# Kernel tuning notes

Hardware: AMD Instinct MI355X
Metric: run time of the kernel (lower is better)

The kernel has to match this reference:

```python
import jax, jax.numpy as jnp
import numpy as np

B, ENC, DEC, H, OUT = 4096, 168, 24, 64, 1
IN = 1 + 5 + 3 + 4 + 7  # 20


def _lstm_step(xt, h, c, Wih, Whh, bih, bhh):
    # PyTorch gate order: i, f, g, o
    g = xt @ Wih.T + h @ Whh.T + bih + bhh
    i, f, gg, o = jnp.split(g, 4, axis=-1)
    c = jax.nn.sigmoid(f) * c + jax.nn.sigmoid(i) * jnp.tanh(gg)
    h = jax.nn.sigmoid(o) * jnp.tanh(c)
    return h, c


def _lstm_layer(x, Wih, Whh, bih, bhh):
    # x: [T, B, in] -> ys: [T, B, H], final (h, c)
    h0 = jnp.zeros((x.shape[1], Whh.shape[1]), x.dtype)

    def step(carry, xt):
        h, c = _lstm_step(xt, carry[0], carry[1], Wih, Whh, bih, bhh)
        return (h, c), h

    (h, c), ys = jax.lax.scan(step, (h0, h0), x)
    return ys, h, c


def setup_inputs() -> dict:
    key = jax.random.key(0)
    ks = jax.random.split(key, 24)
    rn = lambda k, s, sc=0.05: jax.random.normal(k, s, jnp.float32) * sc
    inp = {
        "input_p_q": rn(ks[0], (B, ENC, 1), 1.0),
        "input_time": jax.random.randint(ks[1], (B, ENC, 4), 0, 8),
        "label_p": rn(ks[2], (B, ENC), 1.0),
        "decoder_time": jax.random.randint(ks[3], (B, DEC, 4), 0, 8),
        # encoder LSTM layer 0
        "enc0_Wih": rn(ks[4], (4 * H, IN)), "enc0_Whh": rn(ks[5], (4 * H, H)),
        "enc0_bih": rn(ks[6], (4 * H,)), "enc0_bhh": rn(ks[7], (4 * H,)),
        # encoder LSTM layer 1
        "enc1_Wih": rn(ks[8], (4 * H, H)), "enc1_Whh": rn(ks[9], (4 * H, H)),
        "enc1_bih": rn(ks[10], (4 * H,)), "enc1_bhh": rn(ks[11], (4 * H,)),
        # decoder LSTMCell (input = OUT + 19 = 20)
        "dec_Wih": rn(ks[12], (4 * H, OUT + 19)), "dec_Whh": rn(ks[13], (4 * H, H)),
        "dec_bih": rn(ks[14], (4 * H,)), "dec_bhh": rn(ks[15], (4 * H,)),
        # output projection
        "Wout": rn(ks[16], (OUT, H)), "bout": rn(ks[17], (OUT,)),
        # embeddings
        "emb_hour": rn(ks[18], (24, 5)), "emb_wd": rn(ks[19], (8, 3)),
        "emb_mo": rn(ks[20], (13, 4)), "emb_woy": rn(ks[21], (54, 7)),
    }
    return inp


def reference(input_p_q, input_time, label_p, decoder_time,
              enc0_Wih, enc0_Whh, enc0_bih, enc0_bhh,
              enc1_Wih, enc1_Whh, enc1_bih, enc1_bhh,
              dec_Wih, dec_Whh, dec_bih, dec_bhh,
              Wout, bout, emb_hour, emb_wd, emb_mo, emb_woy):
    def time_feats(t):  # t: [B, T, 4] int -> [B, T, 19]
        return jnp.concatenate([emb_hour[t[:, :, 0]], emb_wd[t[:, :, 1]],
                                emb_mo[t[:, :, 2]], emb_woy[t[:, :, 3]]], axis=-1)

    input_q = label_p[:, :ENC, None]                      # [B, ENC, 1]
    enc_in = jnp.concatenate([input_q, time_feats(input_time)], axis=-1)  # [B, ENC, 20]
    x = enc_in.transpose(1, 0, 2)                         # [ENC, B, 20]
    ys0, _, _ = _lstm_layer(x, enc0_Wih, enc0_Whh, enc0_bih, enc0_bhh)
    _, h1, c1 = _lstm_layer(ys0, enc1_Wih, enc1_Whh, enc1_bih, enc1_bhh)

    dec_feat = time_feats(decoder_time).transpose(1, 0, 2)  # [DEC, B, 19]
    prev0 = label_p[:, ENC - 1, None]                       # [B, 1]

    def dec_step(carry, ft):
        h, c, prev = carry
        xin = jnp.concatenate([prev, ft], axis=-1)          # [B, 20]
        h, c = _lstm_step(xin, h, c, dec_Wih, dec_Whh, dec_bih, dec_bhh)
        out = h @ Wout.T + bout                             # [B, OUT]
        return (h, c, out), out

    _, outs = jax.lax.scan(dec_step, (h1, c1, prev0), dec_feat)
    return outs.transpose(1, 0, 2)                          # [B, DEC, OUT]
```

## Files before the change

### kernel.cpp

```cpp
#include <hip/hip_runtime.h>

#define DEVFN __device__ __forceinline__

typedef float  f32x4  __attribute__((ext_vector_type(4)));
typedef short  bf16x8 __attribute__((ext_vector_type(8)));

constexpr int ENC = 168;
constexpr int DEC = 24;
constexpr int BT  = 16;
constexpr int NBLK = 4096 / BT;

constexpr int W0F = 0;
constexpr int W1F = 24576;
constexpr int WDF = 57344;
constexpr int F_B0   = 40960;
constexpr int F_B1   = 41216;
constexpr int F_BD   = 41472;
constexpr int F_WOUT = 41728;
constexpr int F_BOUT = 41792;
constexpr int F_EMB  = 41793;
constexpr int NEMB = 574;

DEVFN ushort f2bf(float v) {
    unsigned b = __float_as_uint(v);
    return (ushort)((b + 0x7FFFu + ((b >> 16) & 1u)) >> 16);
}
DEVFN float bf2f(ushort u) { return __uint_as_float(((unsigned)u) << 16); }
DEVFN float sigm(float x)  { return __builtin_amdgcn_rcpf(1.f + __expf(-x)); }
DEVFN float tanhv(float x) { return fmaf(2.f, sigm(x + x), -1.f); }

DEVFN unsigned cvt_pk_bf16(float a, float b) {
    unsigned r;
    asm("v_cvt_pk_bf16_f32 %0, %1, %2" : "=v"(r) : "v"(a), "v"(b));
    return r;
}

DEVFN void pinv(bf16x8& v) { asm volatile("" : "+v"(v)); }
DEVFN void pinf(f32x4& v)  { asm volatile("" : "+v"(v)); }

__global__ void prep_kernel(
    const float* __restrict__ w0ih, const float* __restrict__ w0hh,
    const float* __restrict__ b0ih, const float* __restrict__ b0hh,
    const float* __restrict__ w1ih, const float* __restrict__ w1hh,
    const float* __restrict__ b1ih, const float* __restrict__ b1hh,
    const float* __restrict__ wdih, const float* __restrict__ wdhh,
    const float* __restrict__ bdih, const float* __restrict__ bdhh,
    const float* __restrict__ wout, const float* __restrict__ boutp,
    const float* __restrict__ eh,   const float* __restrict__ ewd,
    const float* __restrict__ emo,  const float* __restrict__ ewoy,
    void* __restrict__ ws)
{
    ushort* wsu = (ushort*)ws;
    float*  wsf = (float*)ws;
    const int total = 81920 + 1407;
    for (int idx = blockIdx.x * blockDim.x + threadIdx.x; idx < total;
         idx += gridDim.x * blockDim.x) {
        if (idx < 81920) {
            int layer, q;
            if (idx < W1F)      { layer = 0; q = idx; }
            else if (idx < WDF) { layer = 1; q = idx - W1F; }
            else                { layer = 2; q = idx - WDF; }
            int c  = q >> 13;
            int tt = (q >> 9) & 15;
            int l  = (q >> 3) & 63;
            int j  = q & 7;
            int k  = c * 32 + (l >> 4) * 8 + j;
            int n  = tt * 16 + (l & 15);
            float v = 0.f;
            if (layer == 0) {
                if (k < 20) v = w0ih[n * 20 + k];
                else if (k < 84) v = w0hh[n * 64 + (k - 20)];
            } else if (layer == 1) {
                if (k < 64) v = w1ih[n * 64 + k];
                else        v = w1hh[n * 64 + (k - 64)];
            } else {
                if (k < 20) v = wdih[n * 20 + k];
                else if (k < 84) v = wdhh[n * 64 + (k - 20)];
            }
            wsu[idx] = f2bf(v);
        } else {
            int f = idx - 81920;
            float v;
            if (f < 256)      v = b0ih[f] + b0hh[f];
            else if (f < 512) v = b1ih[f - 256] + b1hh[f - 256];
            else if (f < 768) v = bdih[f - 512] + bdhh[f - 512];
            else if (f < 832) v = wout[f - 768];
            else if (f == 832) v = boutp[0];
            else {
                int e = f - 833;
                if (e < 120)      v = eh[e];
                else if (e < 144) v = ewd[e - 120];
                else if (e < 196) v = emo[e - 144];
                else              v = ewoy[e - 196];
            }
            wsf[40960 + f] = v;
        }
    }
}

DEVFN float emb_lookup(const float* s_emb, int kk, int idx) {
    int f = kk - 1;
    if (f < 5)  return s_emb[idx * 5 + f];
    if (f < 8)  return s_emb[120 + idx * 3 + (f - 5)];
    if (f < 12) return s_emb[144 + idx * 4 + (f - 8)];
    return s_emb[196 + idx * 7 + (f - 12)];
}

DEVFN int offC0(int k, int m) {
    int c = k >> 5, k32 = k & 31;
    return c * 512 + (m + 16 * (k32 >> 3)) * 8 + (k32 & 7);
}
DEVFN int offC3(int k, int m) {
    int c = 3 + (k >> 5), k32 = k & 31;
    return c * 512 + (m + 16 * (k32 >> 3)) * 8 + (k32 & 7);
}
DEVFN void store_h(ushort* A, int off, float h) {
    A[off] = f2bf(h);
}
DEVFN void store_h4(ushort* A, int off, const float* h) {
    unsigned h01 = cvt_pk_bf16(h[0], h[1]);
    unsigned h23 = cvt_pk_bf16(h[2], h[3]);
    asm volatile("" : "+v"(h01), "+v"(h23));
    unsigned long long p = ((unsigned long long)h23 << 32) | h01;
    *(unsigned long long*)(A + off) = p;
}

__global__ __launch_bounds__(512)
__attribute__((amdgpu_waves_per_eu(2, 2)))
void lstm_mfma(
    const int* __restrict__ input_time, const float* __restrict__ label_p,
    const int* __restrict__ decoder_time, const void* __restrict__ ws,
    float* __restrict__ out)
{
    const ushort* wsu = (const ushort*)ws;
    const float*  wsf = (const float*)ws;

    __shared__ __align__(16) ushort Abuf[2][7 * 512];
    __shared__ float s_emb[NEMB];
    __shared__ float s_wout[64];
    __shared__ float sh1[16 * 68];
    __shared__ float s_bout;

    const int tid = threadIdx.x;
    const int w   = tid >> 6;
    const int l   = tid & 63;
    const int q   = l >> 4;
    const int m   = l & 15;
    const int wl  = w & 3;
    const bool isL0 = (w < 4);
    const int b0g = blockIdx.x * BT;
    const int u0  = wl * 16 + q * 4;

    for (int i = tid; i < 2 * 7 * 512; i += 512) ((ushort*)Abuf)[i] = 0;
    for (int i = tid; i < NEMB; i += 512) s_emb[i] = wsf[F_EMB + i];
    if (tid < 64) s_wout[tid] = wsf[F_WOUT + tid];
    if (tid == 0) s_bout = wsf[F_BOUT];

    bf16x8 wA[4][4];
    if (isL0) {
#pragma unroll
        for (int c = 0; c < 3; c++)
#pragma unroll
            for (int g = 0; g < 4; g++)
                wA[c][g] = *(const bf16x8*)(wsu + W0F +
                    (c * 16 + g * 4 + wl) * 512 + l * 8);
        wA[3][0] = wA[3][1] = wA[3][2] = wA[3][3] = bf16x8{0,0,0,0,0,0,0,0};
    } else {
#pragma unroll
        for (int c = 0; c < 4; c++)
#pragma unroll
            for (int g = 0; g < 4; g++)
                wA[c][g] = *(const bf16x8*)(wsu + W1F +
                    (c * 16 + g * 4 + wl) * 512 + l * 8);
    }
#pragma unroll
    for (int c = 0; c < 4; c++)
#pragma unroll
        for (int g = 0; g < 4; g++) pinv(wA[c][g]);

    f32x4 biasv[4];
#pragma unroll
    for (int g = 0; g < 4; g++) {
        biasv[g] = *(const f32x4*)(wsf + (isL0 ? F_B0 : F_B1) + g * 64 + u0);
        pinf(biasv[g]);
    }

    float cst[4] = {0.f, 0.f, 0.f, 0.f};

    const int kk = tid >> 4, mm = tid & 15;
    const bool bx = (tid < 320);
    const int sel = (kk <= 5) ? 0 : (kk <= 8) ? 1 : (kk <= 12) ? 2 : 3;

    __syncthreads();
    if (bx) {
        float v = (kk == 0) ? label_p[(b0g + mm) * ENC]
                : emb_lookup(s_emb, kk, input_time[((b0g + mm) * ENC) * 4 + sel]);
        store_h(Abuf[0], offC0(kk, mm), v);
    }
    __syncthreads();

    for (int i = 0; i <= ENC; ++i) {
        const ushort* Ar = Abuf[i & 1];
        ushort* Aw = Abuf[(i + 1) & 1];
        const bool active = isL0 ? (i < ENC) : (i >= 1);

        float pre_f = 0.f; int pre_i = 0;
        const bool encX  = (i + 1 < ENC) && bx;
        const bool decX0 = (i == ENC) && bx;
        if (encX) {
            if (kk == 0) pre_f = label_p[(b0g + mm) * ENC + (i + 1)];
            else         pre_i = input_time[((b0g + mm) * ENC + (i + 1)) * 4 + sel];
        } else if (decX0) {
            if (kk == 0) pre_f = label_p[(b0g + mm) * ENC + (ENC - 1)];
            else         pre_i = decoder_time[((b0g + mm) * DEC) * 4 + sel];
        }

        if (active) {
            f32x4 acc[4];
#pragma unroll
            for (int g = 0; g < 4; g++) acc[g] = biasv[g];
            if (isL0) {
                bf16x8 ah[3];
#pragma unroll
                for (int c = 0; c < 3; c++)
                    ah[c] = *(const bf16x8*)(Ar + c * 512 + l * 8);
#pragma unroll
                for (int c = 0; c < 3; c++)
#pragma unroll
                    for (int g = 0; g < 4; g++)
                        acc[g] = __builtin_amdgcn_mfma_f32_16x16x32_bf16(
                            wA[c][g], ah[c], acc[g], 0, 0, 0);
            } else {
                bf16x8 ah[4];
#pragma unroll
                for (int c = 0; c < 4; c++)
                    ah[c] = *(const bf16x8*)(Ar + (3 + c) * 512 + l * 8);
#pragma unroll
                for (int c = 0; c < 4; c++)
#pragma unroll
                    for (int g = 0; g < 4; g++)
                        acc[g] = __builtin_amdgcn_mfma_f32_16x16x32_bf16(
                            wA[c][g], ah[c], acc[g], 0, 0, 0);
            }
            float hv[4];
#pragma unroll
            for (int r = 0; r < 4; r++) {
                float cc = sigm(acc[1][r]) * cst[r] + sigm(acc[0][r]) * tanhv(acc[2][r]);
                cst[r] = cc;
                hv[r] = sigm(acc[3][r]) * tanhv(cc);
            }
            if (isL0) {
                store_h4(Aw, offC3(u0, m), hv);
                store_h4(Aw, offC0(20 + u0, m), hv);
            } else {
                if (i < ENC) store_h4(Aw, offC3(64 + u0, m), hv);
                else         store_h4(Aw, offC0(20 + u0, m), hv);
            }
        }
        if (encX || decX0)
            store_h(Aw, offC0(kk, mm), (kk == 0) ? pre_f : emb_lookup(s_emb, kk, pre_i));
        __syncthreads();
    }

    if (!isL0) {
#pragma unroll
        for (int c = 0; c < 3; c++)
#pragma unroll
            for (int g = 0; g < 4; g++)
                wA[c][g] = *(const bf16x8*)(wsu + WDF +
                    (c * 16 + g * 4 + wl) * 512 + l * 8);
#pragma unroll
        for (int c = 0; c < 3; c++)
#pragma unroll
            for (int g = 0; g < 4; g++) pinv(wA[c][g]);
#pragma unroll
        for (int g = 0; g < 4; g++) {
            biasv[g] = *(const f32x4*)(wsf + F_BD + g * 64 + u0);
            pinf(biasv[g]);
        }
    }

    for (int t = 0; t < DEC; ++t) {
        const ushort* Ar = Abuf[(t + 1) & 1];
        ushort* Aw = Abuf[t & 1];

        int pre_i = 0;
        const bool dX = (t + 1 < DEC) && bx && (kk >= 1);
        if (dX) pre_i = decoder_time[((b0g + mm) * DEC + (t + 1)) * 4 + sel];

        if (!isL0) {
            bf16x8 ah[3];
#pragma unroll
            for (int c = 0; c < 3; c++)
                ah[c] = *(const bf16x8*)(Ar + c * 512 + l * 8);
            f32x4 acc[4];
#pragma unroll
            for (int g = 0; g < 4; g++) acc[g] = biasv[g];
#pragma unroll
            for (int c = 0; c < 3; c++)
#pragma unroll
                for (int g = 0; g < 4; g++)
                    acc[g] = __builtin_amdgcn_mfma_f32_16x16x32_bf16(
                        wA[c][g], ah[c], acc[g], 0, 0, 0);
            float hv[4];
#pragma unroll
            for (int r = 0; r < 4; r++) {
                float cc = sigm(acc[1][r]) * cst[r] + sigm(acc[0][r]) * tanhv(acc[2][r]);
                cst[r] = cc;
                hv[r] = sigm(acc[3][r]) * tanhv(cc);
            }
            store_h4(Aw, offC0(20 + u0, m), hv);
            *(f32x4*)&sh1[m * 68 + u0] = *(f32x4*)hv;
        }
        if (dX) store_h(Aw, offC0(kk, mm), emb_lookup(s_emb, kk, pre_i));
        __syncthreads();

        if (tid < 16) {
            float a = s_bout;
#pragma unroll 16
            for (int u = 0; u < 64; u++) a = fmaf(s_wout[u], sh1[tid * 68 + u], a);
            out[(b0g + tid) * DEC + t] = a;
            if (t + 1 < DEC) store_h(Aw, offC0(0, tid), a);
        }
        __syncthreads();
    }
}

extern "C" void kernel_launch(void* const* d_in, const int* in_sizes, int n_in,
                              void* d_out, int out_size, void* d_ws, size_t ws_size,
                              hipStream_t stream)
{
    typedef const float* fp;
    const int* input_time   = (const int*)d_in[1];
    fp         label_p      = (fp)d_in[2];
    const int* decoder_time = (const int*)d_in[3];

    prep_kernel<<<128, 256, 0, stream>>>(
        (fp)d_in[4],  (fp)d_in[5],  (fp)d_in[6],  (fp)d_in[7],
        (fp)d_in[8],  (fp)d_in[9],  (fp)d_in[10], (fp)d_in[11],
        (fp)d_in[12], (fp)d_in[13], (fp)d_in[14], (fp)d_in[15],
        (fp)d_in[16], (fp)d_in[17],
        (fp)d_in[18], (fp)d_in[19], (fp)d_in[20], (fp)d_in[21],
        d_ws);

    lstm_mfma<<<NBLK, 512, 0, stream>>>(
        input_time, label_p, decoder_time, d_ws, (float*)d_out);
}
```

Before: 303.5 us.

## Fold log2e into gate weights, fuse LSTM cell math, share h buffer layout

Gate weights and biases are prescaled by log2(e) (or 2*log2(e) for the g gate) so the activations use raw v_exp_f32 with a negated operand. The sigmoid*tanh products are merged into single reciprocals per gate pair, reducing the exp and rcp count per cell. The shared A buffer is reorganised so the input features get their own 32-wide chunk and each layer writes h only once (one store instead of two for layer 0), shrinking LDS from 7 to 5 chunks. Clamps guard overflow in the fused formulas, but bf16 weight rounding after scaling shifts numerics slightly.

```diff
diff --git a/kernel.cpp b/kernel.cpp
--- a/kernel.cpp
+++ b/kernel.cpp
@@ -9,6 +9,9 @@
 constexpr int DEC = 24;
 constexpr int BT  = 16;
 constexpr int NBLK = 4096 / BT;
+
+constexpr float LOG2E  = 1.4426950408889634f;
+constexpr float LOG2E2 = 2.8853900817779268f;
 
 constexpr int W0F = 0;
 constexpr int W1F = 24576;
@@ -25,18 +28,30 @@
     unsigned b = __float_as_uint(v);
     return (ushort)((b + 0x7FFFu + ((b >> 16) & 1u)) >> 16);
 }
-DEVFN float bf2f(ushort u) { return __uint_as_float(((unsigned)u) << 16); }
-DEVFN float sigm(float x)  { return __builtin_amdgcn_rcpf(1.f + __expf(-x)); }
-DEVFN float tanhv(float x) { return fmaf(2.f, sigm(x + x), -1.f); }
-
 DEVFN unsigned cvt_pk_bf16(float a, float b) {
     unsigned r;
     asm("v_cvt_pk_bf16_f32 %0, %1, %2" : "=v"(r) : "v"(a), "v"(b));
     return r;
 }
-
+DEVFN float exp2n(float x) {
+    float r;
+    asm("v_exp_f32 %0, -%1" : "=v"(r) : "v"(x));
+    return r;
+}
 DEVFN void pinv(bf16x8& v) { asm volatile("" : "+v"(v)); }
 DEVFN void pinf(f32x4& v)  { asm volatile("" : "+v"(v)); }
+
+DEVFN float lstm_cell(float gi, float gf, float gg, float go, float& c) {
+    float a  = exp2n(fmaxf(gi, -21.f));
+    float b  = exp2n(fmaxf(gg, -43.f));
+    float f  = exp2n(gf);
+    float sf = __builtin_amdgcn_rcpf(1.f + f);
+    float it = (1.f - b) * __builtin_amdgcn_rcpf(fmaf(a, b, a + b + 1.f));
+    c = fmaf(sf, c, it);
+    float d  = exp2n(fmaxf(c, -15.f) * LOG2E2);
+    float o  = exp2n(fmaxf(go, -21.f));
+    return (1.f - d) * __builtin_amdgcn_rcpf(fmaf(o, d, o + d + 1.f));
+}
 
 __global__ void prep_kernel(
     const float* __restrict__ w0ih, const float* __restrict__ w0hh,
@@ -69,21 +84,25 @@
             float v = 0.f;
             if (layer == 0) {
                 if (k < 20) v = w0ih[n * 20 + k];
-                else if (k < 84) v = w0hh[n * 64 + (k - 20)];
+                else if (k >= 32 && k < 96) v = w0hh[n * 64 + (k - 32)];
             } else if (layer == 1) {
                 if (k < 64) v = w1ih[n * 64 + k];
                 else        v = w1hh[n * 64 + (k - 64)];
             } else {
                 if (k < 20) v = wdih[n * 20 + k];
-                else if (k < 84) v = wdhh[n * 64 + (k - 20)];
+                else if (k >= 32 && k < 96) v = wdhh[n * 64 + (k - 32)];
             }
+            v *= ((n >> 6) == 2) ? LOG2E2 : LOG2E;
             wsu[idx] = f2bf(v);
         } else {
             int f = idx - 81920;
             float v;
-            if (f < 256)      v = b0ih[f] + b0hh[f];
-            else if (f < 512) v = b1ih[f - 256] + b1hh[f - 256];
-            else if (f < 768) v = bdih[f - 512] + bdhh[f - 512];
+            if (f < 768) {
+                float sc = (((f & 255) >> 6) == 2) ? LOG2E2 : LOG2E;
+                if (f < 256)      v = (b0ih[f] + b0hh[f]) * sc;
+                else if (f < 512) v = (b1ih[f - 256] + b1hh[f - 256]) * sc;
+                else              v = (bdih[f - 512] + bdhh[f - 512]) * sc;
+            }
             else if (f < 832) v = wout[f - 768];
             else if (f == 832) v = boutp[0];
             else {
@@ -105,17 +124,8 @@
     if (f < 12) return s_emb[144 + idx * 4 + (f - 8)];
     return s_emb[196 + idx * 7 + (f - 12)];
 }
-
-DEVFN int offC0(int k, int m) {
-    int c = k >> 5, k32 = k & 31;
-    return c * 512 + (m + 16 * (k32 >> 3)) * 8 + (k32 & 7);
-}
-DEVFN int offC3(int k, int m) {
-    int c = 3 + (k >> 5), k32 = k & 31;
-    return c * 512 + (m + 16 * (k32 >> 3)) * 8 + (k32 & 7);
-}
-DEVFN void store_h(ushort* A, int off, float h) {
-    A[off] = f2bf(h);
+DEVFN int offX(int k, int m) {
+    return (m + 16 * (k >> 3)) * 8 + (k & 7);
 }
 DEVFN void store_h4(ushort* A, int off, const float* h) {
     unsigned h01 = cvt_pk_bf16(h[0], h[1]);
@@ -135,7 +145,7 @@
     const ushort* wsu = (const ushort*)ws;
     const float*  wsf = (const float*)ws;
 
-    __shared__ __align__(16) ushort Abuf[2][7 * 512];
+    __shared__ __align__(16) ushort Abuf[2][5 * 512];
     __shared__ float s_emb[NEMB];
     __shared__ float s_wout[64];
     __shared__ float sh1[16 * 68];
@@ -151,7 +161,11 @@
     const int b0g = blockIdx.x * BT;
     const int u0  = wl * 16 + q * 4;
 
-    for (int i = tid; i < 2 * 7 * 512; i += 512) ((ushort*)Abuf)[i] = 0;
+    const int hoff = (1 + (u0 >> 5)) * 512 +
+                     (m + 16 * ((u0 & 31) >> 3)) * 8 + (u0 & 7) +
+                     (isL0 ? 0 : 1024);
+
+    for (int i = tid; i < 2 * 5 * 512; i += 512) ((ushort*)Abuf)[i] = 0;
     for (int i = tid; i < NEMB; i += 512) s_emb[i] = wsf[F_EMB + i];
     if (tid < 64) s_wout[tid] = wsf[F_WOUT + tid];
     if (tid == 0) s_bout = wsf[F_BOUT];
@@ -187,15 +201,20 @@
 
     float cst[4] = {0.f, 0.f, 0.f, 0.f};
 
-    const int kk = tid >> 4, mm = tid & 15;
-    const bool bx = (tid < 320);
-    const int sel = (kk <= 5) ? 0 : (kk <= 8) ? 1 : (kk <= 12) ? 2 : 3;
+    const int kk1 = tid >> 4;
+    const int sel1 = (kk1 <= 5) ? 0 : (kk1 <= 8) ? 1 : (kk1 <= 12) ? 2 : 3;
+    const int kk2 = kk1 + 16;
+    const bool bx2 = (tid < 64);
 
     __syncthreads();
-    if (bx) {
-        float v = (kk == 0) ? label_p[(b0g + mm) * ENC]
-                : emb_lookup(s_emb, kk, input_time[((b0g + mm) * ENC) * 4 + sel]);
-        store_h(Abuf[0], offC0(kk, mm), v);
+    if (isL0) {
+        float v = (kk1 == 0) ? label_p[(b0g + m) * ENC]
+                : emb_lookup(s_emb, kk1, input_time[((b0g + m) * ENC) * 4 + sel1]);
+        Abuf[0][offX(kk1, m)] = f2bf(v);
+        if (bx2) {
+            float v2 = emb_lookup(s_emb, kk2, input_time[((b0g + m) * ENC) * 4 + 3]);
+            Abuf[0][offX(kk2, m)] = f2bf(v2);
+        }
     }
     __syncthreads();
 
@@ -204,15 +223,17 @@
         ushort* Aw = Abuf[(i + 1) & 1];
         const bool active = isL0 ? (i < ENC) : (i >= 1);
 
-        float pre_f = 0.f; int pre_i = 0;
-        const bool encX  = (i + 1 < ENC) && bx;
-        const bool decX0 = (i == ENC) && bx;
+        float pre_f = 0.f; int pre_i1 = 0, pre_i2 = 0;
+        const bool encX  = (i + 1 < ENC) && isL0;
+        const bool decX0 = (i == ENC) && isL0;
         if (encX) {
-            if (kk == 0) pre_f = label_p[(b0g + mm) * ENC + (i + 1)];
-            else         pre_i = input_time[((b0g + mm) * ENC + (i + 1)) * 4 + sel];
+            if (kk1 == 0) pre_f  = label_p[(b0g + m) * ENC + (i + 1)];
+            else          pre_i1 = input_time[((b0g + m) * ENC + (i + 1)) * 4 + sel1];
+            if (bx2)      pre_i2 = input_time[((b0g + m) * ENC + (i + 1)) * 4 + 3];
         } else if (decX0) {
-            if (kk == 0) pre_f = label_p[(b0g + mm) * ENC + (ENC - 1)];
-            else         pre_i = decoder_time[((b0g + mm) * DEC) * 4 + sel];
+            if (kk1 == 0) pre_f  = label_p[(b0g + m) * ENC + (ENC - 1)];
+            else          pre_i1 = decoder_time[((b0g + m) * DEC) * 4 + sel1];
+            if (bx2)      pre_i2 = decoder_time[((b0g + m) * DEC) * 4 + 3];
         }
 
         if (active) {
@@ -234,7 +255,7 @@
                 bf16x8 ah[4];
 #pragma unroll
                 for (int c = 0; c < 4; c++)
-                    ah[c] = *(const bf16x8*)(Ar + (3 + c) * 512 + l * 8);
+                    ah[c] = *(const bf16x8*)(Ar + (1 + c) * 512 + l * 8);
 #pragma unroll
                 for (int c = 0; c < 4; c++)
 #pragma unroll
@@ -244,21 +265,15 @@
             }
             float hv[4];
 #pragma unroll
-            for (int r = 0; r < 4; r++) {
-                float cc = sigm(acc[1][r]) * cst[r] + sigm(acc[0][r]) * tanhv(acc[2][r]);
-                cst[r] = cc;
-                hv[r] = sigm(acc[3][r]) * tanhv(cc);
-            }
-            if (isL0) {
-                store_h4(Aw, offC3(u0, m), hv);
-                store_h4(Aw, offC0(20 + u0, m), hv);
-            } else {
-                if (i < ENC) store_h4(Aw, offC3(64 + u0, m), hv);
-                else         store_h4(Aw, offC0(20 + u0, m), hv);
-            }
-        }
-        if (encX || decX0)
-            store_h(Aw, offC0(kk, mm), (kk == 0) ? pre_f : emb_lookup(s_emb, kk, pre_i));
+            for (int r = 0; r < 4; r++)
+                hv[r] = lstm_cell(acc[0][r], acc[1][r], acc[2][r], acc[3][r], cst[r]);
+            store_h4(Aw, hoff, hv);
+        }
+        if (encX || decX0) {
+            float v = (kk1 == 0) ? pre_f : emb_lookup(s_emb, kk1, pre_i1);
+            Aw[offX(kk1, m)] = f2bf(v);
+            if (bx2) Aw[offX(kk2, m)] = f2bf(emb_lookup(s_emb, kk2, pre_i2));
+        }
         __syncthreads();
     }
 
@@ -284,15 +299,18 @@
         const ushort* Ar = Abuf[(t + 1) & 1];
         ushort* Aw = Abuf[t & 1];
 
-        int pre_i = 0;
-        const bool dX = (t + 1 < DEC) && bx && (kk >= 1);
-        if (dX) pre_i = decoder_time[((b0g + mm) * DEC + (t + 1)) * 4 + sel];
+        int pre_i1 = 0, pre_i2 = 0;
+        const bool dX = (t + 1 < DEC) && isL0;
+        if (dX) {
+            if (kk1 >= 1) pre_i1 = decoder_time[((b0g + m) * DEC + (t + 1)) * 4 + sel1];
+            if (bx2)      pre_i2 = decoder_time[((b0g + m) * DEC + (t + 1)) * 4 + 3];
+        }
 
         if (!isL0) {
             bf16x8 ah[3];
-#pragma unroll
-            for (int c = 0; c < 3; c++)
-                ah[c] = *(const bf16x8*)(Ar + c * 512 + l * 8);
+            ah[0] = *(const bf16x8*)(Ar + 0 * 512 + l * 8);
+            ah[1] = *(const bf16x8*)(Ar + 3 * 512 + l * 8);
+            ah[2] = *(const bf16x8*)(Ar + 4 * 512 + l * 8);
             f32x4 acc[4];
 #pragma unroll
             for (int g = 0; g < 4; g++) acc[g] = biasv[g];
@@ -304,15 +322,13 @@
                         wA[c][g], ah[c], acc[g], 0, 0, 0);
             float hv[4];
 #pragma unroll
-            for (int r = 0; r < 4; r++) {
-                float cc = sigm(acc[1][r]) * cst[r] + sigm(acc[0][r]) * tanhv(acc[2][r]);
-                cst[r] = cc;
-                hv[r] = sigm(acc[3][r]) * tanhv(cc);
-            }
-            store_h4(Aw, offC0(20 + u0, m), hv);
+            for (int r = 0; r < 4; r++)
+                hv[r] = lstm_cell(acc[0][r], acc[1][r], acc[2][r], acc[3][r], cst[r]);
+            store_h4(Aw, hoff, hv);
             *(f32x4*)&sh1[m * 68 + u0] = *(f32x4*)hv;
         }
-        if (dX) store_h(Aw, offC0(kk, mm), emb_lookup(s_emb, kk, pre_i));
+        if (dX && kk1 >= 1) Aw[offX(kk1, m)] = f2bf(emb_lookup(s_emb, kk1, pre_i1));
+        if (dX && bx2)      Aw[offX(kk2, m)] = f2bf(emb_lookup(s_emb, kk2, pre_i2));
         __syncthreads();
 
         if (tid < 16) {
@@ -320,7 +336,7 @@
 #pragma unroll 16
             for (int u = 0; u < 64; u++) a = fmaf(s_wout[u], sh1[tid * 68 + u], a);
             out[(b0g + tid) * DEC + t] = a;
-            if (t + 1 < DEC) store_h(Aw, offC0(0, tid), a);
+            if (t + 1 < DEC) Aw[offX(0, tid)] = f2bf(a);
         }
         __syncthreads();
     }
```

Result: faster. 287.8 us (-5.2%).
